# Optimization experiments

Hardware: AMD Instinct MI355X
Metric: run time of the kernel (lower is better)

The kernel has to match this reference:

```python
import jax, jax.numpy as jnp
import numpy as np

B, N, C, H = 4, 2048, 256, 16
D = C // H  # head dim = 16


def setup_inputs() -> dict:
    key = jax.random.key(0)
    k1, k2, k3 = jax.random.split(key, 3)
    x = jax.random.normal(k1, (B, N, C), dtype=jnp.float32)
    w_qkv = jax.random.normal(k2, (C, 3 * C), dtype=jnp.float32) * (C ** -0.5)
    b_qkv = jnp.zeros((3 * C,), dtype=jnp.float32)
    w_proj = jax.random.normal(k3, (C, C), dtype=jnp.float32) * (C ** -0.5)
    b_proj = jnp.zeros((C,), dtype=jnp.float32)
    return {"x": x, "w_qkv": w_qkv, "b_qkv": b_qkv, "w_proj": w_proj, "b_proj": b_proj}


def reference(x, w_qkv, b_qkv, w_proj, b_proj):
    b, n, c = x.shape
    qkv = x @ w_qkv + b_qkv                       # (B, N, 3C)
    qkv = qkv.reshape(b, n, 3, H, D)
    q = jnp.transpose(qkv[:, :, 0], (0, 2, 1, 3))  # (B, H, N, D)
    k = jnp.transpose(qkv[:, :, 1], (0, 2, 1, 3))
    v = jnp.transpose(qkv[:, :, 2], (0, 2, 1, 3))
    # NOTE: the original module applies NO 1/sqrt(d) scaling.
    attn = jnp.einsum('bhqd,bhkd->bhqk', q, k)     # (B, H, N, N)
    attn = jax.nn.softmax(attn, axis=-1)
    out = jnp.einsum('bhqk,bhkd->bhqd', attn, v)   # (B, H, N, D)
    out = jnp.transpose(out, (0, 2, 1, 3)).reshape(b, n, c)
    return out @ w_proj + b_proj
```

## Files before the change

### kernel.cpp

```cpp
#include <hip/hip_runtime.h>
#include <stdint.h>

typedef __attribute__((ext_vector_type(8))) short short8;
typedef __attribute__((ext_vector_type(4))) short short4v;
typedef __attribute__((ext_vector_type(4))) float float4v;
typedef __attribute__((ext_vector_type(16))) float float16v;
typedef __attribute__((ext_vector_type(4))) uint32_t uint4v;

__device__ __forceinline__ short f2bf(float f) {
    union { float f; uint32_t u; } v; v.f = f;
    uint32_t u = v.u;
    uint32_t r = (u + 0x7fffu + ((u >> 16) & 1u)) >> 16;
    return (short)r;
}

#if __has_builtin(__builtin_amdgcn_cvt_pk_bf16_f32)
typedef __bf16 bf16x2_t __attribute__((ext_vector_type(2)));
__device__ __forceinline__ uint32_t cvt_pk2(float a, float b) {
    union { bf16x2_t v; uint32_t u; } c;
    c.v = __builtin_amdgcn_cvt_pk_bf16_f32(a, b);
    return c.u;
}
#else
__device__ __forceinline__ uint32_t cvt_pk2(float a, float b) {
    union { float f; uint32_t u; } x, y; x.f = a; y.f = b;
    return ((x.u + 0x8000u) >> 16) | ((y.u + 0x8000u) & 0xFFFF0000u);
}
#endif


__global__ __launch_bounds__(256) void cvtW_kernel(const float* __restrict__ wqkv,
                                                   const float* __restrict__ wproj,
                                                   short* __restrict__ outq,
                                                   short* __restrict__ outp) {
    int idx = blockIdx.x * 256 + threadIdx.x;
    if (idx < 196608) {
        int n = idx >> 8, k = idx & 255;
        outq[idx] = f2bf(wqkv[k * 768 + n]);
    } else {
        int i = idx - 196608;
        int n = i >> 8, k = i & 255;
        outp[i] = f2bf(wproj[k * 256 + n]);
    }
}


template<int MODE>
__global__ __launch_bounds__(256) void gemm_kernel(
    const void* __restrict__ Ap, const short* __restrict__ Bt,
    const float* __restrict__ bias,
    short* __restrict__ outQ, short* __restrict__ outK, short* __restrict__ outV,
    float* __restrict__ outP)
{
    const int K = 256;
    int m0 = blockIdx.x * 64;
    int n0 = blockIdx.y * 64;
    int tid = threadIdx.x;
    int wave = tid >> 6, lane = tid & 63, quad = lane >> 4, lc = lane & 15;

    __shared__ __align__(16) short As[64 * 48];
    __shared__ __align__(16) short Bs[64 * 48];

    float4v acc[4];
    #pragma unroll
    for (int t = 0; t < 4; ++t) acc[t] = (float4v){0.f, 0.f, 0.f, 0.f};

    int srow = tid >> 2, sseg = tid & 3;

    for (int c = 0; c < K; c += 32) {
        __syncthreads();
        if (MODE == 0) {
            const float* src = (const float*)Ap + (size_t)(m0 + srow) * K + c + sseg * 8;
            float4 f0 = *(const float4*)src;
            float4 f1 = *(const float4*)(src + 4);
            uint4v u; u.x = cvt_pk2(f0.x, f0.y); u.y = cvt_pk2(f0.z, f0.w);
            u.z = cvt_pk2(f1.x, f1.y); u.w = cvt_pk2(f1.z, f1.w);
            *(uint4v*)(&As[srow * 48 + sseg * 8]) = u;
        } else {
            *(short8*)(&As[srow * 48 + sseg * 8]) =
                *(const short8*)((const short*)Ap + (size_t)(m0 + srow) * K + c + sseg * 8);
        }
        *(short8*)(&Bs[srow * 48 + sseg * 8]) =
            *(const short8*)(Bt + (size_t)(n0 + srow) * K + c + sseg * 8);
        __syncthreads();

        short8 af = *(short8*)(&As[(wave * 16 + lc) * 48 + quad * 8]);
        #pragma unroll
        for (int t = 0; t < 4; ++t) {
            short8 bf = *(short8*)(&Bs[(t * 16 + lc) * 48 + quad * 8]);
            acc[t] = __builtin_amdgcn_mfma_f32_16x16x32_bf16(af, bf, acc[t], 0, 0, 0);
        }
    }

    #pragma unroll
    for (int t = 0; t < 4; ++t) {
        int cg = n0 + t * 16 + lc;
        float bv = bias[cg];
        #pragma unroll
        for (int r = 0; r < 4; ++r) {
            int rg = m0 + wave * 16 + quad * 4 + r;
            float val = acc[t][r] + bv;
            if (MODE == 0) {
                int s = cg >> 8, rem = cg & 255, h = rem >> 4, d = rem & 15;
                int b = rg >> 11, n = rg & 2047;
                if (s == 0) val *= 1.4426950408889634f;
                short* dst = (s == 0) ? outQ : ((s == 1) ? outK : outV);
                dst[((((size_t)b * 16 + h) * 2048 + n) << 4) + d] = f2bf(val);
            } else {
                outP[(size_t)rg * 256 + cg] = val;
            }
        }
    }
}


__global__ __launch_bounds__(256) void attn_kernel(
    const short* __restrict__ Q, const short* __restrict__ Kp, const short* __restrict__ V,
    short* __restrict__ Out)
{
    const int N = 2048;
    int bh = blockIdx.y;
    int b = bh >> 4, h = bh & 15;
    int tid = threadIdx.x;
    int wave = tid >> 6, lane = tid & 63;
    int m = lane & 31, hi = lane >> 5;
    int qbase = blockIdx.x * 128 + wave * 32;

    const short* Qh = Q + (size_t)bh * N * 16;
    const short* Kh = Kp + (size_t)bh * N * 16;
    const short* Vh = V + (size_t)bh * N * 16;

    __shared__ __align__(16) short Vt[32][264];

    {
        int r = 16 + (tid >> 4);
        int c0 = (tid & 15) * 16;
        short fill = (r == 16) ? (short)0x3F80 : (short)0;
        short8 f8;
        #pragma unroll
        for (int j = 0; j < 8; ++j) f8[j] = fill;
        *(short8*)(&Vt[r][c0]) = f8;
        *(short8*)(&Vt[r][c0 + 8]) = f8;
    }

    short8 qf = *(const short8*)(Qh + (size_t)(qbase + m) * 16 + hi * 8);

    float16v Oacc, zf;
    #pragma unroll
    for (int j = 0; j < 16; ++j) { Oacc[j] = 0.f; zf[j] = 0.f; }

    int sd = tid & 15, sa = tid >> 4;
    int kb = ((sa & 1) << 3) | (((sa >> 1) & 1) << 2) | ((sa >> 2) << 4);

    for (int sc = 0; sc < N; sc += 256) {
        __syncthreads();
        #pragma unroll
        for (int cc = 0; cc < 4; ++cc) {
            const short* vp = Vh + (size_t)(sc + cc * 64 + kb) * 16 + sd;
            short4v pack;
            pack.x = vp[0]; pack.y = vp[16]; pack.z = vp[32]; pack.w = vp[48];
            *(short4v*)(&Vt[sd][cc * 64 + sa * 4]) = pack;
        }
        __syncthreads();

        #pragma unroll
        for (int it = 0; it < 4; ++it) {
            int c = sc + it * 64;
            short8 kf1 = *(const short8*)(Kh + (size_t)(c + m) * 16 + hi * 8);
            short8 kf2 = *(const short8*)(Kh + (size_t)(c + 32 + m) * 16 + hi * 8);

            float16v S1 = __builtin_amdgcn_mfma_f32_32x32x16_bf16(kf1, qf, zf, 0, 0, 0);
            float16v S2 = __builtin_amdgcn_mfma_f32_32x32x16_bf16(kf2, qf, zf, 0, 0, 0);

            union { uint4v u; short8 s; } pA, pB, pC, pD;
            pA.u = (uint4v){
                cvt_pk2(__builtin_amdgcn_exp2f(S1[0]), __builtin_amdgcn_exp2f(S1[1])),
                cvt_pk2(__builtin_amdgcn_exp2f(S1[2]), __builtin_amdgcn_exp2f(S1[3])),
                cvt_pk2(__builtin_amdgcn_exp2f(S1[4]), __builtin_amdgcn_exp2f(S1[5])),
                cvt_pk2(__builtin_amdgcn_exp2f(S1[6]), __builtin_amdgcn_exp2f(S1[7]))};
            pB.u = (uint4v){
                cvt_pk2(__builtin_amdgcn_exp2f(S1[8]),  __builtin_amdgcn_exp2f(S1[9])),
                cvt_pk2(__builtin_amdgcn_exp2f(S1[10]), __builtin_amdgcn_exp2f(S1[11])),
                cvt_pk2(__builtin_amdgcn_exp2f(S1[12]), __builtin_amdgcn_exp2f(S1[13])),
                cvt_pk2(__builtin_amdgcn_exp2f(S1[14]), __builtin_amdgcn_exp2f(S1[15]))};
            pC.u = (uint4v){
                cvt_pk2(__builtin_amdgcn_exp2f(S2[0]), __builtin_amdgcn_exp2f(S2[1])),
                cvt_pk2(__builtin_amdgcn_exp2f(S2[2]), __builtin_amdgcn_exp2f(S2[3])),
                cvt_pk2(__builtin_amdgcn_exp2f(S2[4]), __builtin_amdgcn_exp2f(S2[5])),
                cvt_pk2(__builtin_amdgcn_exp2f(S2[6]), __builtin_amdgcn_exp2f(S2[7]))};
            pD.u = (uint4v){
                cvt_pk2(__builtin_amdgcn_exp2f(S2[8]),  __builtin_amdgcn_exp2f(S2[9])),
                cvt_pk2(__builtin_amdgcn_exp2f(S2[10]), __builtin_amdgcn_exp2f(S2[11])),
                cvt_pk2(__builtin_amdgcn_exp2f(S2[12]), __builtin_amdgcn_exp2f(S2[13])),
                cvt_pk2(__builtin_amdgcn_exp2f(S2[14]), __builtin_amdgcn_exp2f(S2[15]))};

            #pragma unroll
            for (int p = 0; p < 4; ++p) {
                short8 vf = *(const short8*)(&Vt[m][it * 64 + p * 16 + hi * 8]);
                short8 pf = (p == 0) ? pA.s : (p == 1) ? pB.s : (p == 2) ? pC.s : pD.s;
                Oacc = __builtin_amdgcn_mfma_f32_32x32x16_bf16(vf, pf, Oacc, 0, 0, 0);
            }
        }
    }

    float Lq = __shfl(Oacc[8], m, 64);
    float inv = 1.0f / Lq;
    uint32_t o0 = cvt_pk2(Oacc[0] * inv, Oacc[1] * inv);
    uint32_t o1 = cvt_pk2(Oacc[2] * inv, Oacc[3] * inv);
    uint32_t o2 = cvt_pk2(Oacc[4] * inv, Oacc[5] * inv);
    uint32_t o3 = cvt_pk2(Oacc[6] * inv, Oacc[7] * inv);
    short* row = Out + ((size_t)(b * 2048 + qbase + m)) * 256 + h * 16;
    uint2 w0; w0.x = o0; w0.y = o1;
    uint2 w1; w1.x = o2; w1.y = o3;
    *(uint2*)(row + hi * 4) = w0;
    *(uint2*)(row + 8 + hi * 4) = w1;
}


extern "C" void kernel_launch(void* const* d_in, const int* in_sizes, int n_in,
                              void* d_out, int out_size, void* d_ws, size_t ws_size,
                              hipStream_t stream) {
    const float* x      = (const float*)d_in[0];
    const float* w_qkv  = (const float*)d_in[1];
    const float* b_qkv  = (const float*)d_in[2];
    const float* w_proj = (const float*)d_in[3];
    const float* b_proj = (const float*)d_in[4];
    float* out = (float*)d_out;

    short* wqkvT  = (short*)d_ws;
    short* wprojT = wqkvT + 196608;
    short* Qb     = wprojT + 65536;
    short* Kb     = Qb + 2097152;
    short* Vb     = Kb + 2097152;
    short* Ab     = Vb + 2097152;

    cvtW_kernel<<<1024, 256, 0, stream>>>(w_qkv, w_proj, wqkvT, wprojT);

    gemm_kernel<0><<<dim3(128, 12), 256, 0, stream>>>(x, wqkvT, b_qkv, Qb, Kb, Vb, nullptr);

    attn_kernel<<<dim3(16, 64), 256, 0, stream>>>(Qb, Kb, Vb, Ab);

    gemm_kernel<1><<<dim3(128, 4), 256, 0, stream>>>(Ab, wprojT, b_proj,
                                                     nullptr, nullptr, nullptr, out);
}
```

Baseline: 139.9 us.

## Prefetch V and K tiles into registers and shrink shared V buffer

The attention kernel now loads the next 256-key V chunk into registers while the current chunk is in use, and loads K fragments for the next 64-key step right after the score MFMAs instead of just before them. This is meant to hide global-load latency behind compute. The shared V tile is halved to 16 rows, and the constant ones and zeros rows used to build the row-sum are supplied from registers by lane selection instead of shared memory. The cost is more live registers and a per-lane branch in the inner loop.

```diff
diff --git a/kernel.cpp b/kernel.cpp
--- a/kernel.cpp
+++ b/kernel.cpp
@@ -101,10 +101,10 @@
             int rg = m0 + wave * 16 + quad * 4 + r;
             float val = acc[t][r] + bv;
             if (MODE == 0) {
-                int s = cg >> 8, rem = cg & 255, h = rem >> 4, d = rem & 15;
+                int sq = cg >> 8, rem = cg & 255, h = rem >> 4, d = rem & 15;
                 int b = rg >> 11, n = rg & 2047;
-                if (s == 0) val *= 1.4426950408889634f;
-                short* dst = (s == 0) ? outQ : ((s == 1) ? outK : outV);
+                if (sq == 0) val *= 1.4426950408889634f;
+                short* dst = (sq == 0) ? outQ : ((sq == 1) ? outK : outV);
                 dst[((((size_t)b * 16 + h) * 2048 + n) << 4) + d] = f2bf(val);
             } else {
                 outP[(size_t)rg * 256 + cg] = val;
@@ -130,20 +130,13 @@
     const short* Kh = Kp + (size_t)bh * N * 16;
     const short* Vh = V + (size_t)bh * N * 16;
 
-    __shared__ __align__(16) short Vt[32][264];
-
-    {
-        int r = 16 + (tid >> 4);
-        int c0 = (tid & 15) * 16;
-        short fill = (r == 16) ? (short)0x3F80 : (short)0;
-        short8 f8;
-        #pragma unroll
-        for (int j = 0; j < 8; ++j) f8[j] = fill;
-        *(short8*)(&Vt[r][c0]) = f8;
-        *(short8*)(&Vt[r][c0 + 8]) = f8;
-    }
+    __shared__ __align__(16) short Vt[16][264];
 
     short8 qf = *(const short8*)(Qh + (size_t)(qbase + m) * 16 + hi * 8);
+
+    short8 ones, zeros;
+    #pragma unroll
+    for (int j = 0; j < 8; ++j) { ones[j] = (short)0x3F80; zeros[j] = 0; }
 
     float16v Oacc, zf;
     #pragma unroll
@@ -152,25 +145,42 @@
     int sd = tid & 15, sa = tid >> 4;
     int kb = ((sa & 1) << 3) | (((sa >> 1) & 1) << 2) | ((sa >> 2) << 4);
 
+    short4v vpack[4];
+    #pragma unroll
+    for (int cc = 0; cc < 4; ++cc) {
+        const short* vp = Vh + (size_t)(cc * 64 + kb) * 16 + sd;
+        vpack[cc].x = vp[0]; vpack[cc].y = vp[16];
+        vpack[cc].z = vp[32]; vpack[cc].w = vp[48];
+    }
+
+    short8 kf1 = *(const short8*)(Kh + (size_t)m * 16 + hi * 8);
+    short8 kf2 = *(const short8*)(Kh + (size_t)(32 + m) * 16 + hi * 8);
+
     for (int sc = 0; sc < N; sc += 256) {
         __syncthreads();
         #pragma unroll
-        for (int cc = 0; cc < 4; ++cc) {
-            const short* vp = Vh + (size_t)(sc + cc * 64 + kb) * 16 + sd;
-            short4v pack;
-            pack.x = vp[0]; pack.y = vp[16]; pack.z = vp[32]; pack.w = vp[48];
-            *(short4v*)(&Vt[sd][cc * 64 + sa * 4]) = pack;
+        for (int cc = 0; cc < 4; ++cc)
+            *(short4v*)(&Vt[sd][cc * 64 + sa * 4]) = vpack[cc];
+        if (sc + 256 < N) {
+            #pragma unroll
+            for (int cc = 0; cc < 4; ++cc) {
+                const short* vp = Vh + (size_t)(sc + 256 + cc * 64 + kb) * 16 + sd;
+                vpack[cc].x = vp[0]; vpack[cc].y = vp[16];
+                vpack[cc].z = vp[32]; vpack[cc].w = vp[48];
+            }
         }
         __syncthreads();
 
         #pragma unroll
         for (int it = 0; it < 4; ++it) {
             int c = sc + it * 64;
-            short8 kf1 = *(const short8*)(Kh + (size_t)(c + m) * 16 + hi * 8);
-            short8 kf2 = *(const short8*)(Kh + (size_t)(c + 32 + m) * 16 + hi * 8);
+            int cn = (c + 64) & (N - 1);
 
             float16v S1 = __builtin_amdgcn_mfma_f32_32x32x16_bf16(kf1, qf, zf, 0, 0, 0);
             float16v S2 = __builtin_amdgcn_mfma_f32_32x32x16_bf16(kf2, qf, zf, 0, 0, 0);
+
+            kf1 = *(const short8*)(Kh + (size_t)(cn + m) * 16 + hi * 8);
+            kf2 = *(const short8*)(Kh + (size_t)(cn + 32 + m) * 16 + hi * 8);
 
             union { uint4v u; short8 s; } pA, pB, pC, pD;
             pA.u = (uint4v){
@@ -196,7 +206,10 @@
 
             #pragma unroll
             for (int p = 0; p < 4; ++p) {
-                short8 vf = *(const short8*)(&Vt[m][it * 64 + p * 16 + hi * 8]);
+                short8 vf;
+                if (m < 16)      vf = *(const short8*)(&Vt[m][it * 64 + p * 16 + hi * 8]);
+                else if (m == 16) vf = ones;
+                else              vf = zeros;
                 short8 pf = (p == 0) ? pA.s : (p == 1) ? pB.s : (p == 2) ? pC.s : pD.s;
                 Oacc = __builtin_amdgcn_mfma_f32_32x32x16_bf16(vf, pf, Oacc, 0, 0, 0);
             }
```

Measured after the change: 134.1 us, median of 2. 1.04x faster.
